# Optimization experiments

Hardware: AMD Instinct MI355X
Metric: run time of the kernel (lower is better)

Reference implementation:

```python
import jax, jax.numpy as jnp
import numpy as np

N_USERS = 100000
N_ITEMS = 50000
N_NODES = N_USERS + N_ITEMS
NNZ = 4000000
DIM = 64
N_LAYERS = 3
BATCH = 4096


def setup_inputs() -> dict:
    key = jax.random.key(0)
    k = jax.random.split(key, 7)
    users = jax.random.randint(k[0], (BATCH,), 0, N_USERS, dtype=jnp.int32)
    items = jax.random.randint(k[1], (BATCH,), 0, N_ITEMS, dtype=jnp.int32)
    edge_src = jax.random.randint(k[2], (NNZ,), 0, N_NODES, dtype=jnp.int32)
    edge_dst = jax.random.randint(k[3], (NNZ,), 0, N_NODES, dtype=jnp.int32)
    # normalized adjacency values (positive weights, like D^-1/2 A D^-1/2)
    edge_val = jax.random.uniform(k[4], (NNZ,), dtype=jnp.float32)
    user_emb = 0.1 * jax.random.normal(k[5], (N_USERS, DIM), dtype=jnp.float32)
    item_emb = 0.1 * jax.random.normal(k[6], (N_ITEMS, DIM), dtype=jnp.float32)
    return {"users": users, "items": items, "edge_src": edge_src,
            "edge_dst": edge_dst, "edge_val": edge_val,
            "user_emb": user_emb, "item_emb": item_emb}


def _spmm(edge_src, edge_dst, edge_val, emb):
    # y[dst] += val * emb[src]  (sparse adjacency @ dense embedding)
    vals = edge_val[:, None] * emb[edge_src]          # [nnz, d]
    return jax.ops.segment_sum(vals, edge_dst, num_segments=N_NODES)


def reference(users, items, edge_src, edge_dst, edge_val, user_emb, item_emb):
    all_emb = jnp.concatenate([user_emb, item_emb], axis=0)  # [N, d]
    acc = all_emb
    x = all_emb
    for _ in range(N_LAYERS):
        x = _spmm(edge_src, edge_dst, edge_val, x)
        acc = acc + x
    light_out = acc / jnp.asarray(N_LAYERS + 1, dtype=acc.dtype)  # layer mean
    all_users = light_out[:N_USERS]
    all_items = light_out[N_USERS:]
    u = all_users[users]                              # [B, d]
    i = all_items[items]                              # [B, d]
    scores = jnp.sum(u * i, axis=-1)                  # [B]
    return jax.nn.sigmoid(scores)
```

## Files before the change

### kernel.cpp

```cpp
#include <hip/hip_runtime.h>
#include <hip/hip_fp16.h>

#define N_USERS 100000
#define N_ITEMS 50000
#define N_NODES 150000
#define DIM 64
#define NNZ 4000000
#define BATCH 4096

#define NBUCK 586
#define CAP   7680
#define NB_C  256
#define CHUNK (NNZ / NB_C)

typedef __half f16;

__device__ __forceinline__ float h2f(f16 h) { return __half2float(h); }

__global__ void initt_k(int* __restrict__ gticket) {
    int i = blockIdx.x * blockDim.x + threadIdx.x;
    if (i < NBUCK) gticket[i] = i * CAP;
}

__global__ __launch_bounds__(1024) void coarse_k(
        const int* __restrict__ src, const int* __restrict__ dst,
        const float* __restrict__ val, int* __restrict__ gticket,
        int2* __restrict__ ev) {
    extern __shared__ char smem[];
    int2* buf   = (int2*)smem;
    int*  hist  = (int*)(smem + (size_t)CHUNK * 8);
    int*  lbase = hist  + NBUCK;
    int*  gbase = lbase + NBUCK;
    int*  tick  = gbase + NBUCK;
    const int t  = threadIdx.x;
    const int nt = blockDim.x;
    const int lo = blockIdx.x * CHUNK;
    const int hi = lo + CHUNK;

    for (int i = t; i < NBUCK; i += nt) { hist[i] = 0; tick[i] = 0; }
    __syncthreads();
    for (int e = lo + t; e < hi; e += nt)
        atomicAdd(&hist[dst[e] >> 8], 1);
    __syncthreads();
    if (t < 64) {
        int lane = t;
        int carry = 0;
        for (int c = 0; c < (NBUCK + 63) / 64; ++c) {
            int idx = c * 64 + lane;
            int v = (idx < NBUCK) ? hist[idx] : 0;
            int s = v;
            #pragma unroll
            for (int off = 1; off < 64; off <<= 1) {
                int u = __shfl_up(s, off, 64);
                if (lane >= off) s += u;
            }
            if (idx < NBUCK) lbase[idx] = carry + s - v;
            carry += __shfl(s, 63, 64);
        }
    }
    for (int i = t; i < NBUCK; i += nt)
        gbase[i] = atomicAdd(&gticket[i], hist[i]);
    __syncthreads();
    for (int e = lo + t; e < hi; e += nt) {
        int d  = dst[e];
        int bk = d >> 8;
        int p  = lbase[bk] + atomicAdd(&tick[bk], 1);
        buf[p] = make_int2(src[e] | ((d & 255) << 18), __float_as_int(val[e]));
    }
    __syncthreads();
    int wid = t >> 6, lane = t & 63, nw = nt >> 6;
    for (int bk = wid; bk < NBUCK; bk += nw) {
        int cnt = hist[bk], lb = lbase[bk], gb = gbase[bk];
        for (int i = lane; i < cnt; i += 64)
            ev[gb + i] = buf[lb + i];
    }
}

__global__ void scanC_k(const int* __restrict__ gticket, int* __restrict__ bktbase) {
    __shared__ int sh[1024];
    int tid = threadIdx.x;
    int v = (tid < NBUCK) ? (gticket[tid] - tid * CAP) : 0;
    sh[tid] = v;
    __syncthreads();
    for (int off = 1; off < 1024; off <<= 1) {
        int t = (tid >= off) ? sh[tid - off] : 0;
        __syncthreads();
        sh[tid] += t;
        __syncthreads();
    }
    if (tid < NBUCK) bktbase[tid] = sh[tid] - v;
}

__global__ void fine_k(const int* __restrict__ gticket, const int* __restrict__ bktbase,
                       const int2* __restrict__ ev,
                       int2* __restrict__ sorted, int* __restrict__ row) {
    __shared__ int hist[256];
    __shared__ int sh[256];
    int k = blockIdx.x, t = threadIdx.x;
    hist[t] = 0;
    __syncthreads();
    int cnt = gticket[k] - k * CAP;
    int s0  = k * CAP;
    for (int i = t; i < cnt; i += 256)
        atomicAdd(&hist[(ev[s0 + i].x >> 18) & 255], 1);
    __syncthreads();
    int v = hist[t];
    sh[t] = v;
    __syncthreads();
    for (int off = 1; off < 256; off <<= 1) {
        int tmp = (t >= off) ? sh[t - off] : 0;
        __syncthreads();
        sh[t] += tmp;
        __syncthreads();
    }
    int excl    = sh[t] - v;
    int rowbase = bktbase[k];
    int node    = (k << 8) + t;
    if (node < N_NODES) row[node] = rowbase + excl;
    if (k == 0 && t == 0) row[N_NODES] = NNZ;
    hist[t] = excl;
    __syncthreads();
    for (int i = t; i < cnt; i += 256) {
        int2 r = ev[s0 + i];
        int p  = atomicAdd(&hist[(r.x >> 18) & 255], 1);
        sorted[rowbase + p] = make_int2(r.x & 0x3FFFF, r.y);
    }
}

__global__ void conv_k(const float4* __restrict__ ue, const float4* __restrict__ ie,
                       ushort4* __restrict__ X0) {
    int i = blockIdx.x * blockDim.x + threadIdx.x;
    const int total  = N_NODES * DIM / 4;
    const int ubound = N_USERS * DIM / 4;
    if (i >= total) return;
    float4 v = (i < ubound) ? ue[i] : ie[i - ubound];
    f16 a = __float2half(v.x), b = __float2half(v.y);
    f16 c = __float2half(v.z), d = __float2half(v.w);
    ushort4 o;
    o.x = *reinterpret_cast<ushort*>(&a);
    o.y = *reinterpret_cast<ushort*>(&b);
    o.z = *reinterpret_cast<ushort*>(&c);
    o.w = *reinterpret_cast<ushort*>(&d);
    X0[i] = o;
}

__global__ void gather16_k(const int* __restrict__ row, const int2* __restrict__ se,
                           const uint2* __restrict__ X4, uint2* __restrict__ Y4) {
    int wid  = (blockIdx.x * blockDim.x + threadIdx.x) >> 6;
    int lane = threadIdx.x & 63;
    if (wid >= N_NODES) return;
    int sub  = lane >> 4;
    int quad = lane & 15;
    int beg = row[wid], end = row[wid + 1];
    float a0 = 0.f, a1 = 0.f, a2 = 0.f, a3 = 0.f;
    for (int base = beg; base < end; base += 64) {
        int rem = end - base;
        int n = rem < 64 ? rem : 64;
        int2 evv = make_int2(0, 0);
        if (lane < n) evv = se[base + lane];
        int ng = (n + 3) >> 2;
        for (int g0 = 0; g0 < ng; g0 += 4) {
            uint2 xr[4]; float vs[4];
            #pragma unroll
            for (int k = 0; k < 4; ++k) {
                int ei = ((g0 + k) << 2) + sub;
                int sx = __shfl(evv.x, ei, 64);
                vs[k]  = __int_as_float(__shfl(evv.y, ei, 64));
                xr[k]  = X4[((size_t)sx << 4) + quad];
            }
            #pragma unroll
            for (int k = 0; k < 4; ++k) {
                float2 f0 = __half22float2(*reinterpret_cast<const half2*>(&xr[k].x));
                float2 f1 = __half22float2(*reinterpret_cast<const half2*>(&xr[k].y));
                a0 += vs[k] * f0.x;
                a1 += vs[k] * f0.y;
                a2 += vs[k] * f1.x;
                a3 += vs[k] * f1.y;
            }
        }
    }
    a0 += __shfl_xor(a0, 16, 64);  a1 += __shfl_xor(a1, 16, 64);
    a2 += __shfl_xor(a2, 16, 64);  a3 += __shfl_xor(a3, 16, 64);
    a0 += __shfl_xor(a0, 32, 64);  a1 += __shfl_xor(a1, 32, 64);
    a2 += __shfl_xor(a2, 32, 64);  a3 += __shfl_xor(a3, 32, 64);
    if (sub == 0) {
        half2 h0 = __floats2half2_rn(a0, a1);
        half2 h1 = __floats2half2_rn(a2, a3);
        uint2 o;
        o.x = *reinterpret_cast<uint*>(&h0);
        o.y = *reinterpret_cast<uint*>(&h1);
        Y4[((size_t)wid << 4) + quad] = o;
    }
}

__global__ void gather3_k(const int* __restrict__ users, const int* __restrict__ items,
                          const int* __restrict__ row, const int2* __restrict__ se,
                          const f16* __restrict__ X, f16* __restrict__ X3p) {
    int s    = (blockIdx.x * blockDim.x + threadIdx.x) >> 6;
    int lane = threadIdx.x & 63;
    if (s >= 2 * BATCH) return;
    int wid = (s < BATCH) ? users[s] : (N_USERS + items[s - BATCH]);
    int beg = row[wid], end = row[wid + 1];
    float acc = 0.f;
    for (int base = beg; base < end; base += 64) {
        int rem = end - base;
        int n = rem < 64 ? rem : 64;
        int2 evv = make_int2(0, 0);
        if (lane < n) evv = se[base + lane];
        int n8 = (n + 7) & ~7;
        for (int j = 0; j < n8; j += 8) {
            float xv[8], vv[8];
            #pragma unroll
            for (int k = 0; k < 8; ++k) {
                int sr = __shfl(evv.x, j + k, 64);
                vv[k] = __int_as_float(__shfl(evv.y, j + k, 64));
                xv[k] = h2f(X[(sr << 6) + lane]);
            }
            #pragma unroll
            for (int k = 0; k < 8; ++k) acc += vv[k] * xv[k];
        }
    }
    X3p[(s << 6) + lane] = __float2half(acc);
}

__global__ void final_k(const int* __restrict__ users, const int* __restrict__ items,
                        const float* __restrict__ ue, const float* __restrict__ ie,
                        const f16* __restrict__ X1, const f16* __restrict__ X2,
                        const f16* __restrict__ X3p, float* __restrict__ out) {
    int b    = blockIdx.x * (blockDim.x / 64) + (threadIdx.x / 64);
    int lane = threadIdx.x & 63;
    if (b >= BATCH) return;
    int u  = users[b];
    int it = items[b];
    int uo = (u << 6) + lane;
    int io = ((N_USERS + it) << 6) + lane;
    float au = ue[uo]               + h2f(X1[uo]) + h2f(X2[uo]) + h2f(X3p[(b << 6) + lane]);
    float ai = ie[(it << 6) + lane] + h2f(X1[io]) + h2f(X2[io]) + h2f(X3p[((b + BATCH) << 6) + lane]);
    float p = au * ai * (1.0f / 16.0f);
    #pragma unroll
    for (int off = 32; off; off >>= 1) p += __shfl_down(p, off, 64);
    if (lane == 0) out[b] = 1.0f / (1.0f + __expf(-p));
}

extern "C" void kernel_launch(void* const* d_in, const int* in_sizes, int n_in,
                              void* d_out, int out_size, void* d_ws, size_t ws_size,
                              hipStream_t stream) {
    const int*   users = (const int*)  d_in[0];
    const int*   items = (const int*)  d_in[1];
    const int*   esrc  = (const int*)  d_in[2];
    const int*   edst  = (const int*)  d_in[3];
    const float* eval  = (const float*)d_in[4];
    const float* uemb  = (const float*)d_in[5];
    const float* iemb  = (const float*)d_in[6];
    float*       out   = (float*)      d_out;

    const size_t XB = (size_t)N_NODES * DIM * sizeof(f16);
    char* ws = (char*)d_ws;
    f16*  X0     = (f16*) (ws);
    f16*  X1     = (f16*) (ws + XB);
    f16*  X2     = (f16*) (ws + 2 * XB);
    f16*  X3p    = (f16*) (ws + 3 * XB);
    int2* sorted = (int2*)(ws + 3 * XB + ((size_t)2 * BATCH * DIM * 2 + 255 & ~255UL));
    char* p      = (char*)sorted + (size_t)NNZ * sizeof(int2);
    int*  row     = (int*)(p);                 p += ((size_t)(N_NODES + 1) * 4 + 255) & ~255UL;
    int*  gticket = (int*)(p);                 p += (NBUCK * 4 + 255) & ~255UL;
    int*  bktbase = (int*)(p);
    int2* cev = (int2*)(ws);

    const size_t CLDS = (size_t)CHUNK * 8 + (size_t)4 * NBUCK * 4;
    hipFuncSetAttribute((const void*)coarse_k,
                        hipFuncAttributeMaxDynamicSharedMemorySize, (int)CLDS);

    initt_k<<<(NBUCK + 255) / 256, 256, 0, stream>>>(gticket);
    coarse_k<<<NB_C, 1024, CLDS, stream>>>(esrc, edst, eval, gticket, cev);
    scanC_k<<<1, 1024, 0, stream>>>(gticket, bktbase);
    fine_k<<<NBUCK, 256, 0, stream>>>(gticket, bktbase, cev, sorted, row);

    conv_k<<<(N_NODES * DIM / 4 + 255) / 256, 256, 0, stream>>>(
        (const float4*)uemb, (const float4*)iemb, (ushort4*)X0);

    const int gthreads = N_NODES * 64;
    gather16_k<<<(gthreads + 255) / 256, 256, 0, stream>>>(row, sorted,
                                                           (const uint2*)X0, (uint2*)X1);
    gather16_k<<<(gthreads + 255) / 256, 256, 0, stream>>>(row, sorted,
                                                           (const uint2*)X1, (uint2*)X2);
    gather3_k<<<(2 * BATCH * 64 + 255) / 256, 256, 0, stream>>>(users, items, row,
                                                                sorted, X2, X3p);

    final_k<<<(BATCH * 64 + 255) / 256, 256, 0, stream>>>(users, items, uemb, iemb,
                                                          X1, X2, X3p, out);
}
```

Measured before the change: 234.0 us.

## Vectorize edge bucketing loads and accumulate SpMM in packed half2 FMA

The coarse bucketing kernel now reads dst/src/val two elements at a time through int2/float2 loads. NB_C changes from 256 to 250 so CHUNK divides NNZ evenly and stays even, which the pairwise loads need. The SpMM gather kernel replaces its fp32 accumulation with packed half2 FMA, which cuts conversions and ALU work. Accumulating in fp16 over rows with about 27 edges each carries accuracy risk, since rounding error and possible overflow can build up across the three layers.

Result: faster. 226.9 us (-3.1%).

```diff
diff --git a/kernel.cpp b/kernel.cpp
--- a/kernel.cpp
+++ b/kernel.cpp
@@ -10,7 +10,7 @@
 
 #define NBUCK 586
 #define CAP   7680
-#define NB_C  256
+#define NB_C  250
 #define CHUNK (NNZ / NB_C)
 
 typedef __half f16;
@@ -39,8 +39,11 @@
 
     for (int i = t; i < NBUCK; i += nt) { hist[i] = 0; tick[i] = 0; }
     __syncthreads();
-    for (int e = lo + t; e < hi; e += nt)
-        atomicAdd(&hist[dst[e] >> 8], 1);
+    for (int e = lo + 2 * t; e < hi; e += 2 * nt) {
+        int2 d2 = *reinterpret_cast<const int2*>(&dst[e]);
+        atomicAdd(&hist[d2.x >> 8], 1);
+        atomicAdd(&hist[d2.y >> 8], 1);
+    }
     __syncthreads();
     if (t < 64) {
         int lane = t;
@@ -61,11 +64,16 @@
     for (int i = t; i < NBUCK; i += nt)
         gbase[i] = atomicAdd(&gticket[i], hist[i]);
     __syncthreads();
-    for (int e = lo + t; e < hi; e += nt) {
-        int d  = dst[e];
-        int bk = d >> 8;
-        int p  = lbase[bk] + atomicAdd(&tick[bk], 1);
-        buf[p] = make_int2(src[e] | ((d & 255) << 18), __float_as_int(val[e]));
+    for (int e = lo + 2 * t; e < hi; e += 2 * nt) {
+        int2   d2 = *reinterpret_cast<const int2*>(&dst[e]);
+        int2   s2 = *reinterpret_cast<const int2*>(&src[e]);
+        float2 v2 = *reinterpret_cast<const float2*>(&val[e]);
+        int bk0 = d2.x >> 8;
+        int p0  = lbase[bk0] + atomicAdd(&tick[bk0], 1);
+        buf[p0] = make_int2(s2.x | ((d2.x & 255) << 18), __float_as_int(v2.x));
+        int bk1 = d2.y >> 8;
+        int p1  = lbase[bk1] + atomicAdd(&tick[bk1], 1);
+        buf[p1] = make_int2(s2.y | ((d2.y & 255) << 18), __float_as_int(v2.y));
     }
     __syncthreads();
     int wid = t >> 6, lane = t & 63, nw = nt >> 6;
@@ -152,7 +160,8 @@
     int sub  = lane >> 4;
     int quad = lane & 15;
     int beg = row[wid], end = row[wid + 1];
-    float a0 = 0.f, a1 = 0.f, a2 = 0.f, a3 = 0.f;
+    half2 acc0 = __floats2half2_rn(0.f, 0.f);
+    half2 acc1 = acc0;
     for (int base = beg; base < end; base += 64) {
         int rem = end - base;
         int n = rem < 64 ? rem : 64;
@@ -170,15 +179,15 @@
             }
             #pragma unroll
             for (int k = 0; k < 4; ++k) {
-                float2 f0 = __half22float2(*reinterpret_cast<const half2*>(&xr[k].x));
-                float2 f1 = __half22float2(*reinterpret_cast<const half2*>(&xr[k].y));
-                a0 += vs[k] * f0.x;
-                a1 += vs[k] * f0.y;
-                a2 += vs[k] * f1.x;
-                a3 += vs[k] * f1.y;
+                half2 vh = __float2half2_rn(vs[k]);
+                acc0 = __hfma2(*reinterpret_cast<half2*>(&xr[k].x), vh, acc0);
+                acc1 = __hfma2(*reinterpret_cast<half2*>(&xr[k].y), vh, acc1);
             }
         }
     }
+    float2 f0 = __half22float2(acc0);
+    float2 f1 = __half22float2(acc1);
+    float a0 = f0.x, a1 = f0.y, a2 = f1.x, a3 = f1.y;
     a0 += __shfl_xor(a0, 16, 64);  a1 += __shfl_xor(a1, 16, 64);
     a2 += __shfl_xor(a2, 16, 64);  a3 += __shfl_xor(a3, 16, 64);
     a0 += __shfl_xor(a0, 32, 64);  a1 += __shfl_xor(a1, 32, 64);
```

## Vectorize bucketing loads, widen gather unroll, add nontemporal loads/stores

Applied to the files above, without the earlier changes.

The coarse bucketing kernel now reads dst/src/val as int4/float4 and handles four edges per thread per iteration. NB_C changes from 256 to 250 so that CHUNK (16000) stays divisible by 4 for those vector loads. The SpMM gather kernel unrolls from 4 to 8 row gathers per group to keep more loads in flight, and uses nontemporal hints for the edge-list loads and the output stores. More registers per thread may lower occupancy, and with ng not always a multiple of 8 the extra iterations shuffle out-of-range lanes. Those lanes carry zero values, so results stay correct at the cost of some wasted loads.

Result: slower. 241.1 us (+3.0%).

```diff
diff --git a/kernel.cpp b/kernel.cpp
--- a/kernel.cpp
+++ b/kernel.cpp
@@ -10,7 +10,7 @@
 
 #define NBUCK 586
 #define CAP   7680
-#define NB_C  256
+#define NB_C  250
 #define CHUNK (NNZ / NB_C)
 
 typedef __half f16;
@@ -39,8 +39,13 @@
 
     for (int i = t; i < NBUCK; i += nt) { hist[i] = 0; tick[i] = 0; }
     __syncthreads();
-    for (int e = lo + t; e < hi; e += nt)
-        atomicAdd(&hist[dst[e] >> 8], 1);
+    for (int e = lo + 4 * t; e < hi; e += 4 * nt) {
+        int4 d4 = *reinterpret_cast<const int4*>(&dst[e]);
+        atomicAdd(&hist[d4.x >> 8], 1);
+        atomicAdd(&hist[d4.y >> 8], 1);
+        atomicAdd(&hist[d4.z >> 8], 1);
+        atomicAdd(&hist[d4.w >> 8], 1);
+    }
     __syncthreads();
     if (t < 64) {
         int lane = t;
@@ -61,11 +66,19 @@
     for (int i = t; i < NBUCK; i += nt)
         gbase[i] = atomicAdd(&gticket[i], hist[i]);
     __syncthreads();
-    for (int e = lo + t; e < hi; e += nt) {
-        int d  = dst[e];
-        int bk = d >> 8;
-        int p  = lbase[bk] + atomicAdd(&tick[bk], 1);
-        buf[p] = make_int2(src[e] | ((d & 255) << 18), __float_as_int(val[e]));
+    for (int e = lo + 4 * t; e < hi; e += 4 * nt) {
+        int4   d4 = *reinterpret_cast<const int4*>(&dst[e]);
+        int4   s4 = *reinterpret_cast<const int4*>(&src[e]);
+        float4 v4 = *reinterpret_cast<const float4*>(&val[e]);
+        int bk, p;
+        bk = d4.x >> 8; p = lbase[bk] + atomicAdd(&tick[bk], 1);
+        buf[p] = make_int2(s4.x | ((d4.x & 255) << 18), __float_as_int(v4.x));
+        bk = d4.y >> 8; p = lbase[bk] + atomicAdd(&tick[bk], 1);
+        buf[p] = make_int2(s4.y | ((d4.y & 255) << 18), __float_as_int(v4.y));
+        bk = d4.z >> 8; p = lbase[bk] + atomicAdd(&tick[bk], 1);
+        buf[p] = make_int2(s4.z | ((d4.z & 255) << 18), __float_as_int(v4.z));
+        bk = d4.w >> 8; p = lbase[bk] + atomicAdd(&tick[bk], 1);
+        buf[p] = make_int2(s4.w | ((d4.w & 255) << 18), __float_as_int(v4.w));
     }
     __syncthreads();
     int wid = t >> 6, lane = t & 63, nw = nt >> 6;
@@ -157,19 +170,23 @@
         int rem = end - base;
         int n = rem < 64 ? rem : 64;
         int2 evv = make_int2(0, 0);
-        if (lane < n) evv = se[base + lane];
+        if (lane < n) {
+            long long tmp = __builtin_nontemporal_load(
+                reinterpret_cast<const long long*>(&se[base + lane]));
+            evv = *reinterpret_cast<int2*>(&tmp);
+        }
         int ng = (n + 3) >> 2;
-        for (int g0 = 0; g0 < ng; g0 += 4) {
-            uint2 xr[4]; float vs[4];
-            #pragma unroll
-            for (int k = 0; k < 4; ++k) {
+        for (int g0 = 0; g0 < ng; g0 += 8) {
+            uint2 xr[8]; float vs[8];
+            #pragma unroll
+            for (int k = 0; k < 8; ++k) {
                 int ei = ((g0 + k) << 2) + sub;
                 int sx = __shfl(evv.x, ei, 64);
                 vs[k]  = __int_as_float(__shfl(evv.y, ei, 64));
                 xr[k]  = X4[((size_t)sx << 4) + quad];
             }
             #pragma unroll
-            for (int k = 0; k < 4; ++k) {
+            for (int k = 0; k < 8; ++k) {
                 float2 f0 = __half22float2(*reinterpret_cast<const half2*>(&xr[k].x));
                 float2 f1 = __half22float2(*reinterpret_cast<const half2*>(&xr[k].y));
                 a0 += vs[k] * f0.x;
@@ -189,7 +206,8 @@
         uint2 o;
         o.x = *reinterpret_cast<uint*>(&h0);
         o.y = *reinterpret_cast<uint*>(&h1);
-        Y4[((size_t)wid << 4) + quad] = o;
+        __builtin_nontemporal_store(*reinterpret_cast<unsigned long long*>(&o),
+            reinterpret_cast<unsigned long long*>(&Y4[((size_t)wid << 4) + quad]));
     }
 }
 
```
